# Kernel optimization log

Measured on AMD Instinct MI355X. Metric: run time of the kernel, lower is better.

The kernel has to match this reference:

```python
import jax, jax.numpy as jnp
import numpy as np
import math

B, S, HID = 1, 2048, 4096
NH, NKV, HD = 32, 8, 128
N_REP = NH // NKV
ROPE_THETA = 10000.0


def setup_inputs() -> dict:
    key = jax.random.key(0)
    ks = jax.random.split(key, 5)
    hidden_states = jax.random.normal(ks[0], (B, S, HID), dtype=jnp.float32)
    # additive causal mask: 0 on/below diagonal, -1e9 above
    causal = jnp.triu(jnp.full((S, S), -1e9, dtype=jnp.float32), k=1)
    attention_mask = causal[None, None, :, :]
    wq = jax.random.normal(ks[1], (HID, NH * HD), dtype=jnp.float32) * 0.02
    wk = jax.random.normal(ks[2], (HID, NKV * HD), dtype=jnp.float32) * 0.02
    wv = jax.random.normal(ks[3], (HID, NKV * HD), dtype=jnp.float32) * 0.02
    wo = jax.random.normal(ks[4], (NH * HD, HID), dtype=jnp.float32) * 0.02
    return {"hidden_states": hidden_states, "attention_mask": attention_mask,
            "wq": wq, "wk": wk, "wv": wv, "wo": wo}


def _rope_cos_sin(seq_len, head_dim, base, dtype):
    inv_freq = 1.0 / (base ** (jnp.arange(0, head_dim, 2, dtype=jnp.float32) / head_dim))
    t = jnp.arange(seq_len, dtype=jnp.float32)
    freqs = jnp.outer(t, inv_freq)          # [S, HD/2]
    emb = jnp.concatenate([freqs, freqs], axis=-1)  # [S, HD]
    return jnp.cos(emb).astype(dtype), jnp.sin(emb).astype(dtype)


def _rotate_interleaved(x):
    # pairs (x0,x1) -> (-x1, x0), interleaved (matches torch stack/reshape trick)
    xp = x.reshape(*x.shape[:-1], -1, 2)
    return jnp.stack([-xp[..., 1], xp[..., 0]], axis=-1).reshape(x.shape)


def reference(hidden_states, attention_mask, wq, wk, wv, wo):
    b, s, _ = hidden_states.shape
    q = (hidden_states @ wq).reshape(b, s, NH, HD).transpose(0, 2, 1, 3)   # [B,NH,S,HD]
    k = (hidden_states @ wk).reshape(b, s, NKV, HD).transpose(0, 2, 1, 3)  # [B,NKV,S,HD]
    v = (hidden_states @ wv).reshape(b, s, NKV, HD).transpose(0, 2, 1, 3)

    cos, sin = _rope_cos_sin(s, HD, ROPE_THETA, hidden_states.dtype)
    cos = cos[None, None, :, :]  # broadcast over batch and heads
    sin = sin[None, None, :, :]
    q = q * cos + _rotate_interleaved(q) * sin
    k = k * cos + _rotate_interleaved(k) * sin

    # repeat_kv: [B,NKV,S,HD] -> [B,NH,S,HD]
    k = jnp.repeat(k, N_REP, axis=1)
    v = jnp.repeat(v, N_REP, axis=1)

    scores = jnp.einsum('bhqd,bhkd->bhqk', q, k) / math.sqrt(HD)
    scores = scores + attention_mask
    attn = jax.nn.softmax(scores.astype(jnp.float32), axis=-1).astype(q.dtype)
    out = jnp.einsum('bhqk,bhkd->bhqd', attn, v)          # [B,NH,S,HD]
    out = out.transpose(0, 2, 1, 3).reshape(b, s, NH * HD)
    return out @ wo
```

## Files before the change

### kernel.cpp

```cpp
#include <hip/hip_runtime.h>

#define S_LEN 2048
#define HID 4096
#define NH 32
#define NKV 8
#define HD 128
#define KVW 1024
#define NQKV 6144

typedef _Float16 f16;
typedef _Float16 f16x8 __attribute__((ext_vector_type(8)));
typedef _Float16 f16x4 __attribute__((ext_vector_type(4)));
typedef float f32x4 __attribute__((ext_vector_type(4)));
typedef float f32x16 __attribute__((ext_vector_type(16)));
typedef unsigned int u32;
typedef u32 u32x4 __attribute__((ext_vector_type(4)));

__device__ __forceinline__ void gll16(const void* g, void* lds) {
  __builtin_amdgcn_global_load_lds((const __attribute__((address_space(1))) void*)g,
                                   (__attribute__((address_space(3))) void*)lds, 16, 0, 0);
}

template<int N> __device__ __forceinline__ void vmwait() {
  if constexpr (N == 0) asm volatile("s_waitcnt vmcnt(0)" ::: "memory");
  else if constexpr (N == 2) asm volatile("s_waitcnt vmcnt(2)" ::: "memory");
  else if constexpr (N == 3) asm volatile("s_waitcnt vmcnt(3)" ::: "memory");
  else if constexpr (N == 4) asm volatile("s_waitcnt vmcnt(4)" ::: "memory");
  else if constexpr (N == 6) asm volatile("s_waitcnt vmcnt(6)" ::: "memory");
  else static_assert(N == 0, "add vmcnt case");
}

__global__ void k_cast(const float* __restrict__ src, f16* __restrict__ dst) {
  size_t i = ((size_t)blockIdx.x * blockDim.x + threadIdx.x) * 8;
  float4 a = *(const float4*)(src + i);
  float4 b = *(const float4*)(src + i + 4);
  f16x8 o = { (f16)a.x, (f16)a.y, (f16)a.z, (f16)a.w,
              (f16)b.x, (f16)b.y, (f16)b.z, (f16)b.w };
  *(f16x8*)(dst + i) = o;
}

__global__ void k_trig(float4* __restrict__ trig) {
  int id = blockIdx.x * blockDim.x + threadIdx.x;
  int s = id >> 6, i = id & 63;
  int j0 = 2 * i, j1 = 2 * i + 1;
  float f0 = powf(10000.f, -(float)(j0 & 63) / 64.f);
  float f1 = powf(10000.f, -(float)(j1 & 63) / 64.f);
  float a0 = (float)s * f0, a1 = (float)s * f1;
  trig[id] = make_float4(cosf(a0), cosf(a1), sinf(a0), sinf(a1));
}

__global__ __launch_bounds__(256) void k_wprep(
    const float* __restrict__ wq, const float* __restrict__ wk,
    const float* __restrict__ wv, const float* __restrict__ wo,
    f16* __restrict__ Wt, f16* __restrict__ Wot)
{
  __shared__ float tile[32][33];
  int bid = blockIdx.x;
  const float* src; f16* dst; int N; int r;
  if (bid < 16384)      { src = wq; dst = Wt;                          N = 4096; r = bid; }
  else if (bid < 20480) { src = wk; dst = Wt + (size_t)4096 * 4096;    N = 1024; r = bid - 16384; }
  else if (bid < 24576) { src = wv; dst = Wt + (size_t)5120 * 4096;    N = 1024; r = bid - 20480; }
  else                  { src = wo; dst = Wot;                         N = 4096; r = bid - 24576; }
  int tpr = N >> 5;
  int kb = (r / tpr) * 32, nb = (r % tpr) * 32;
  int t = threadIdx.x;
  {
    int kl = t >> 3, ng = t & 7;
    float4 v = *(const float4*)(src + (size_t)(kb + kl) * N + nb + ng * 4);
    tile[kl][ng * 4 + 0] = v.x; tile[kl][ng * 4 + 1] = v.y;
    tile[kl][ng * 4 + 2] = v.z; tile[kl][ng * 4 + 3] = v.w;
  }
  __syncthreads();
  {
    int nl = t >> 3, kg = t & 7;
    f16x4 o = { (f16)tile[kg * 4 + 0][nl], (f16)tile[kg * 4 + 1][nl],
                (f16)tile[kg * 4 + 2][nl], (f16)tile[kg * 4 + 3][nl] };
    *(f16x4*)(dst + (size_t)(nb + nl) * HID + kb + kg * 4) = o;
  }
}

extern __shared__ char smem[];

template<int MODE, int MF, int NF, int WM, int WN>
__global__ __launch_bounds__(WM * WN * 64, 2) void k_gemm4(
    const f16* __restrict__ A, const f16* __restrict__ Bt,
    f16* __restrict__ Qr, f16* __restrict__ Kr, f16* __restrict__ Vt,
    const float4* __restrict__ trig, float* __restrict__ Cout)
{
  constexpr int NTHR = WM * WN * 64;
  constexpr int BM = WM * MF * 16;
  constexpr int BN = WN * NF * 16;
  constexpr int ABYTES = BM * 128;
  constexpr int BBYTES = BN * 128;
  constexpr int RPC = NTHR / 8;
  constexpr int ACALLS = BM / RPC;
  constexpr int BCALLS = BN / RPC;
  constexpr int NT = 64;

  const int tid = threadIdx.x, ln = tid & 63, w = tid >> 6;
  const int la = ln & 15, lg = ln >> 4;
  const int wr = w / WN, wc = w % WN;

  int bx, by;
  {
    int b = blockIdx.y * gridDim.x + blockIdx.x;
    int cx = gridDim.x >> 3;
    int xcd = b & 7, rr = b >> 3;
    bx = xcd * cx + (rr % cx);
    by = rr / cx;
  }
  const int m0 = by * BM, n0 = bx * BN;

  const char* asrc[ACALLS];
  const char* bsrc[BCALLS];
  int adst[ACALLS > BCALLS ? ACALLS : BCALLS];
#pragma unroll
  for (int c = 0; c < ACALLS; ++c) {
    int r = c * RPC + (tid >> 3);
    int g = (tid & 7) ^ (r & 7);
    asrc[c] = (const char*)A + ((size_t)(m0 + r) * HID + (size_t)g * 8) * 2;
    adst[c] = c * NTHR * 16 + tid * 16;
  }
#pragma unroll
  for (int c = 0; c < BCALLS; ++c) {
    int r = c * RPC + (tid >> 3);
    int g = (tid & 7) ^ (r & 7);
    bsrc[c] = (const char*)Bt + ((size_t)(n0 + (r >= BN ? r - BN : r)) * HID + (size_t)g * 8) * 2;
  }

  char* const Bbase = smem + 2 * ABYTES;
  f32x4 acc[MF][NF] = {};

#pragma unroll
  for (int c = 0; c < ACALLS; ++c) gll16(asrc[c], smem + adst[c]);
#pragma unroll
  for (int c = 0; c < BCALLS; ++c) gll16(bsrc[c], Bbase + adst[c]);
#pragma unroll
  for (int c = 0; c < BCALLS; ++c) gll16(bsrc[c] + 128, Bbase + 1 * BBYTES + adst[c]);
#pragma unroll
  for (int c = 0; c < BCALLS; ++c) gll16(bsrc[c] + 256, Bbase + 2 * BBYTES + adst[c]);
  vmwait<2 * BCALLS>();
  __builtin_amdgcn_s_barrier();

  for (int t = 0; t < NT; ++t) {
    if (t + 1 < NT) {
      char* sa = smem + ((t + 1) & 1) * ABYTES;
#pragma unroll
      for (int c = 0; c < ACALLS; ++c) gll16(asrc[c] + (size_t)(t + 1) * 128, sa + adst[c]);
    }
    if (t + 3 < NT) {
      char* sb = Bbase + ((t + 3) & 3) * BBYTES;
#pragma unroll
      for (int c = 0; c < BCALLS; ++c) gll16(bsrc[c] + (size_t)(t + 3) * 128, sb + adst[c]);
    }
    const char* sa = smem + (t & 1) * ABYTES;
    const char* sb = Bbase + (t & 3) * BBYTES;
#pragma unroll
    for (int ks = 0; ks < 2; ++ks) {
      f16x8 af[MF], bf[NF];
#pragma unroll
      for (int i = 0; i < MF; ++i) {
        int rl = wr * MF * 16 + i * 16 + la;
        af[i] = *(const f16x8*)(sa + rl * 128 + (((ks * 4 + lg) ^ (rl & 7)) * 16));
      }
#pragma unroll
      for (int n = 0; n < NF; ++n) {
        int rb = wc * NF * 16 + n * 16 + la;
        bf[n] = *(const f16x8*)(sb + rb * 128 + (((ks * 4 + lg) ^ (rb & 7)) * 16));
      }
      __builtin_amdgcn_s_setprio(1);
#pragma unroll
      for (int i = 0; i < MF; ++i)
#pragma unroll
        for (int n = 0; n < NF; ++n)
          acc[i][n] = __builtin_amdgcn_mfma_f32_16x16x32_f16(af[i], bf[n], acc[i][n], 0, 0, 0);
      __builtin_amdgcn_s_setprio(0);
    }
    if (t < NT - 3)      vmwait<BCALLS>();
    else if (t < NT - 1) vmwait<0>();
    if (t < NT - 1) __builtin_amdgcn_s_barrier();
  }

#pragma unroll
  for (int mi = 0; mi < MF; ++mi) {
#pragma unroll
    for (int nf = 0; nf < NF; ++nf) {
      f32x4 fr = acc[mi][nf];
      int n = n0 + wc * NF * 16 + nf * 16 + la;
      int mr = m0 + wr * MF * 16 + mi * 16 + lg * 4;
      if (MODE == 0) {
        if (n < HID + KVW) {
          int d = n & 127;
#pragma unroll
          for (int r = 0; r < 4; ++r) {
            float v = fr[r];
            float p = __shfl_xor(v, 1);
            float4 tc = trig[(size_t)(mr + r) * 64 + (d >> 1)];
            float cv = (d & 1) ? tc.y : tc.x;
            float sv = (d & 1) ? tc.w : tc.z;
            float o = v * cv + ((d & 1) ? p : -p) * sv;
            if (n < HID) Qr[(size_t)(mr + r) * HID + n] = (f16)o;
            else         Kr[(size_t)(mr + r) * KVW + (n - HID)] = (f16)o;
          }
        } else {
          int nv = n - (HID + KVW);
          f16x4 o4 = { (f16)fr[0], (f16)fr[1], (f16)fr[2], (f16)fr[3] };
          *(f16x4*)(Vt + (size_t)nv * S_LEN + mr) = o4;
        }
      } else {
#pragma unroll
        for (int r = 0; r < 4; ++r)
          Cout[(size_t)(mr + r) * HID + n] = fr[r];
      }
    }
  }
}

#define KBYTES (64 * 128 * 2)
#define VBYTES (128 * 64 * 2)

__global__ __launch_bounds__(256, 2) void k_attn(
    const f16* __restrict__ Qr, const f16* __restrict__ Kr, const f16* __restrict__ Vt,
    f16* __restrict__ AO)
{
  int bid = blockIdx.x;
  int h, c;
  if (bid < 256) { h = bid >> 3; c = bid & 7; }
  else           { int t = bid - 256; h = t >> 3; c = 15 - (t & 7); }
  const int hkv = h >> 2;
  const int q0c = c * 128;
  const int NT = 2 * c + 2;

  __shared__ char KV[2][KBYTES + VBYTES];

  const int tid = threadIdx.x;
  const int ln = tid & 63, w = tid >> 6;
  const int q = ln & 31;
  const int hi = ln >> 5;
  const int qg = q0c + w * 32 + q;

  size_t ksrc[4], vsrc[4];
  int kdo[4], vdo[4];
#pragma unroll
  for (int j = 0; j < 4; ++j) {
    int kc = w * 4 + j;
    int kr = kc * 4 + (ln >> 4);
    ksrc[j] = ((size_t)kr * KVW + hkv * HD) * 2 + (size_t)(((ln & 15) ^ (kr & 7)) * 16);
    kdo[j] = kc * 1024;
    int vc = w * 4 + j;
    int d = vc * 8 + (ln >> 3);
    vsrc[j] = ((size_t)(hkv * HD + d) * S_LEN) * 2 + (size_t)(((ln & 7) ^ (d & 7)) * 16);
    vdo[j] = KBYTES + vc * 1024;
  }

  f16x8 qf[8];
  {
    const f16* qrow = Qr + (size_t)qg * HID + h * HD + hi * 8;
#pragma unroll
    for (int ks = 0; ks < 8; ++ks) qf[ks] = *(const f16x8*)(qrow + ks * 16);
  }

  f32x16 ot[4] = {};
  float m2 = -3.0e38f, l = 0.f;
  const float K2 = 0.12753256471f;

  int buf = 0;
#pragma unroll
  for (int j = 0; j < 4; ++j) {
    gll16((const char*)Kr + ksrc[j], &KV[0][kdo[j]]);
    gll16((const char*)Vt + vsrc[j], &KV[0][vdo[j]]);
  }

  for (int jt = 0; jt < NT; ++jt) {
    __syncthreads();
    if (jt + 1 < NT) {
      size_t ko = (size_t)(jt + 1) * 64 * KVW * 2;
      size_t vo = (size_t)(jt + 1) * 64 * 2;
#pragma unroll
      for (int j = 0; j < 4; ++j) {
        gll16((const char*)Kr + ksrc[j] + ko, &KV[buf ^ 1][kdo[j]]);
        gll16((const char*)Vt + vsrc[j] + vo, &KV[buf ^ 1][vdo[j]]);
      }
    }
    const int j0 = jt * 64;
    if (j0 <= q0c + w * 32 + 31) {
      const f16* Kb = (const f16*)&KV[buf][0];
      const f16* Vb = (const f16*)&KV[buf][KBYTES];
      f32x16 s0 = {}, s1 = {};
#pragma unroll
      for (int ks = 0; ks < 8; ++ks) {
        int cc = ((ks * 2 + hi) ^ (q & 7)) * 8;
        f16x8 k0 = *(const f16x8*)(Kb + q * 128 + cc);
        f16x8 k1 = *(const f16x8*)(Kb + (q + 32) * 128 + cc);
        s0 = __builtin_amdgcn_mfma_f32_32x32x16_f16(k0, qf[ks], s0, 0, 0, 0);
        s1 = __builtin_amdgcn_mfma_f32_32x32x16_f16(k1, qf[ks], s1, 0, 0, 0);
      }
      const bool nm = (j0 + 63 > q0c + w * 32);
      float p0[16], p1[16];
      float mx = -3.0e38f;
#pragma unroll
      for (int r = 0; r < 16; ++r) {
        float a = s0[r], b = s1[r];
        if (nm) {
          int kvb = j0 + (r & 3) + 8 * (r >> 2) + 4 * hi;
          if (kvb > qg) a = -3.0e38f;
          if (kvb + 32 > qg) b = -3.0e38f;
        }
        p0[r] = a; p1[r] = b;
        mx = fmaxf(mx, fmaxf(a, b));
      }
      mx = fmaxf(mx, __shfl_xor(mx, 32));
      float m2c = mx * K2;
      int defer = (m2c <= m2 + 11.0f);
      if (!__all(defer)) {
        float m2n = fmaxf(m2, m2c);
        float corr = exp2f(m2 - m2n);
        m2 = m2n; l *= corr;
#pragma unroll
        for (int t = 0; t < 4; ++t)
#pragma unroll
          for (int r = 0; r < 16; ++r) ot[t][r] *= corr;
      }
      float sum = 0.f;
#pragma unroll
      for (int r = 0; r < 16; ++r) {
        p0[r] = exp2f(__builtin_fmaf(p0[r], K2, -m2));
        p1[r] = exp2f(__builtin_fmaf(p1[r], K2, -m2));
        sum += p0[r] + p1[r];
      }
      l += sum + __shfl_xor(sum, 32);
      u32 pw0[8], pw1[8];
#pragma unroll
      for (int t = 0; t < 8; ++t) {
        pw0[t] = __builtin_bit_cast(u32, __builtin_amdgcn_cvt_pkrtz(p0[2 * t], p0[2 * t + 1]));
        pw1[t] = __builtin_bit_cast(u32, __builtin_amdgcn_cvt_pkrtz(p1[2 * t], p1[2 * t + 1]));
      }
      f16x8 pf[4];
#pragma unroll
      for (int ch = 0; ch < 2; ++ch) {
        const u32* pw = ch ? pw1 : pw0;
        u32 sx[8];
#pragma unroll
        for (int t = 0; t < 8; ++t) sx[t] = (u32)__shfl_xor((int)pw[t], 32);
        u32x4 fa = { hi ? sx[2] : pw[0], hi ? sx[3] : pw[1],
                     hi ? pw[2] : sx[0], hi ? pw[3] : sx[1] };
        u32x4 fb = { hi ? sx[6] : pw[4], hi ? sx[7] : pw[5],
                     hi ? pw[6] : sx[4], hi ? pw[7] : sx[5] };
        pf[ch * 2 + 0] = __builtin_bit_cast(f16x8, fa);
        pf[ch * 2 + 1] = __builtin_bit_cast(f16x8, fb);
      }
#pragma unroll
      for (int dt = 0; dt < 4; ++dt) {
        int d = dt * 32 + q;
#pragma unroll
        for (int f = 0; f < 4; ++f) {
          f16x8 vf = *(const f16x8*)(Vb + d * 64 + (((f * 2 + hi) ^ (q & 7)) * 8));
          ot[dt] = __builtin_amdgcn_mfma_f32_32x32x16_f16(vf, pf[f], ot[dt], 0, 0, 0);
        }
      }
    }
    buf ^= 1;
  }

  __syncthreads();
  char* scr = &KV[0][0] + w * 8192;
  float inv = 1.f / l;
#pragma unroll
  for (int dt = 0; dt < 4; ++dt) {
#pragma unroll
    for (int rg = 0; rg < 4; ++rg) {
      u32 wa = __builtin_bit_cast(u32, __builtin_amdgcn_cvt_pkrtz(ot[dt][rg * 4 + 0] * inv, ot[dt][rg * 4 + 1] * inv));
      u32 wb = __builtin_bit_cast(u32, __builtin_amdgcn_cvt_pkrtz(ot[dt][rg * 4 + 2] * inv, ot[dt][rg * 4 + 3] * inv));
      int byte = q * 256 + (((dt * 4 + rg) ^ (q & 7)) * 16) + hi * 8;
      u32* p = (u32*)(scr + byte);
      p[0] = wa; p[1] = wb;
    }
  }
  asm volatile("s_waitcnt lgkmcnt(0)" ::: "memory");
#pragma unroll
  for (int ps = 0; ps < 8; ++ps) {
    int qr = ps * 4 + (ln >> 4);
    int ck = (ln & 15) ^ (qr & 7);
    f16x8 v = *(const f16x8*)(scr + qr * 256 + ck * 16);
    *(f16x8*)(AO + (size_t)(q0c + w * 32 + qr) * HID + h * HD + (ln & 15) * 8) = v;
  }
}

extern "C" void kernel_launch(void* const* d_in, const int* in_sizes, int n_in,
                              void* d_out, int out_size, void* d_ws, size_t ws_size,
                              hipStream_t stream) {
  const float* hs = (const float*)d_in[0];
  const float* wq = (const float*)d_in[2];
  const float* wk = (const float*)d_in[3];
  const float* wv = (const float*)d_in[4];
  const float* wo = (const float*)d_in[5];
  float* out = (float*)d_out;

  char* ws = (char*)d_ws;
  size_t off = 0;
  auto alloc = [&](size_t b) { char* p = ws + off; off += (b + 255) & ~(size_t)255; return p; };
  f16* Hh   = (f16*)alloc((size_t)S_LEN * HID * 2);
  f16* Wt   = (f16*)alloc((size_t)NQKV * HID * 2);
  float4* trig = (float4*)alloc((size_t)S_LEN * 64 * sizeof(float4));
  f16* Qrp  = (f16*)alloc((size_t)S_LEN * HID * 2);
  f16* Krp  = (f16*)alloc((size_t)S_LEN * KVW * 2);
  f16* Vtp  = (f16*)alloc((size_t)KVW * S_LEN * 2);
  f16* AO   = (f16*)alloc((size_t)S_LEN * HID * 2);
  f16* Wot  = (f16*)alloc((size_t)HID * HID * 2);

  hipFuncSetAttribute((const void*)k_gemm4<0, 8, 3, 2, 4>,
                      hipFuncAttributeMaxDynamicSharedMemorySize, 163840);
  hipFuncSetAttribute((const void*)k_gemm4<1, 8, 2, 2, 4>,
                      hipFuncAttributeMaxDynamicSharedMemorySize, 131072);

  k_cast<<<(S_LEN * HID) / (256 * 8), 256, 0, stream>>>(hs, Hh);
  k_trig<<<(S_LEN * 64) / 256, 256, 0, stream>>>(trig);
  k_wprep<<<40960, 256, 0, stream>>>(wq, wk, wv, wo, Wt, Wot);
  k_gemm4<0, 8, 3, 2, 4><<<dim3(NQKV / 192, S_LEN / 256), 512, 163840, stream>>>(
      Hh, Wt, Qrp, Krp, Vtp, trig, nullptr);
  k_attn<<<dim3(512), 256, 0, stream>>>(Qrp, Krp, Vtp, AO);
  k_gemm4<1, 8, 2, 2, 4><<<dim3(HID / 128, S_LEN / 256), 512, 131072, stream>>>(
      AO, Wot, nullptr, nullptr, nullptr, nullptr, out);
}
```

Measured before the change: 322.5 us.

## Add finer-grained pipelined QKV GEMM kernel and fuse prep kernels into one launch

Replaces the templated QKV projection GEMM with a dedicated kernel that splits each K-tile into half-k stages. It uses a 4-slot A ring and a 3-slot B ring, interleaves global-to-LDS loads between MFMA sub-blocks with more barriers, and remaps blocks per XCD for locality. It also merges the cast, trig and weight-transpose kernels into a single launch to cut launch overhead. LDS per block drops, but the extra barriers and finer vmcnt waits may stall waves.

```diff
diff --git a/kernel.cpp b/kernel.cpp
--- a/kernel.cpp
+++ b/kernel.cpp
@@ -26,36 +26,44 @@
   else if constexpr (N == 2) asm volatile("s_waitcnt vmcnt(2)" ::: "memory");
   else if constexpr (N == 3) asm volatile("s_waitcnt vmcnt(3)" ::: "memory");
   else if constexpr (N == 4) asm volatile("s_waitcnt vmcnt(4)" ::: "memory");
+  else if constexpr (N == 5) asm volatile("s_waitcnt vmcnt(5)" ::: "memory");
   else if constexpr (N == 6) asm volatile("s_waitcnt vmcnt(6)" ::: "memory");
+  else if constexpr (N == 7) asm volatile("s_waitcnt vmcnt(7)" ::: "memory");
+  else if constexpr (N == 8) asm volatile("s_waitcnt vmcnt(8)" ::: "memory");
   else static_assert(N == 0, "add vmcnt case");
 }
-
-__global__ void k_cast(const float* __restrict__ src, f16* __restrict__ dst) {
-  size_t i = ((size_t)blockIdx.x * blockDim.x + threadIdx.x) * 8;
-  float4 a = *(const float4*)(src + i);
-  float4 b = *(const float4*)(src + i + 4);
-  f16x8 o = { (f16)a.x, (f16)a.y, (f16)a.z, (f16)a.w,
-              (f16)b.x, (f16)b.y, (f16)b.z, (f16)b.w };
-  *(f16x8*)(dst + i) = o;
-}
-
-__global__ void k_trig(float4* __restrict__ trig) {
-  int id = blockIdx.x * blockDim.x + threadIdx.x;
-  int s = id >> 6, i = id & 63;
-  int j0 = 2 * i, j1 = 2 * i + 1;
-  float f0 = powf(10000.f, -(float)(j0 & 63) / 64.f);
-  float f1 = powf(10000.f, -(float)(j1 & 63) / 64.f);
-  float a0 = (float)s * f0, a1 = (float)s * f1;
-  trig[id] = make_float4(cosf(a0), cosf(a1), sinf(a0), sinf(a1));
-}
-
-__global__ __launch_bounds__(256) void k_wprep(
-    const float* __restrict__ wq, const float* __restrict__ wk,
-    const float* __restrict__ wv, const float* __restrict__ wo,
-    f16* __restrict__ Wt, f16* __restrict__ Wot)
+#define LGKM0 asm volatile("s_waitcnt lgkmcnt(0)" ::: "memory")
+#define BAR() __builtin_amdgcn_s_barrier()
+
+__global__ __launch_bounds__(256) void k_prep(
+    const float* __restrict__ hs, const float* __restrict__ wq,
+    const float* __restrict__ wk, const float* __restrict__ wv,
+    const float* __restrict__ wo,
+    f16* __restrict__ Hh, f16* __restrict__ Wt, f16* __restrict__ Wot,
+    float4* __restrict__ trig)
 {
   __shared__ float tile[32][33];
   int bid = blockIdx.x;
+  int t = threadIdx.x;
+  if (bid >= 40960) {
+    int b2 = bid - 40960;
+    if (b2 < 4096) {
+      size_t i = ((size_t)b2 * 256 + t) * 8;
+      float4 a = *(const float4*)(hs + i);
+      float4 b = *(const float4*)(hs + i + 4);
+      f16x8 o = { (f16)a.x, (f16)a.y, (f16)a.z, (f16)a.w,
+                  (f16)b.x, (f16)b.y, (f16)b.z, (f16)b.w };
+      *(f16x8*)(Hh + i) = o;
+    } else {
+      int id = (b2 - 4096) * 256 + t;
+      int s = id >> 6, i = id & 63;
+      float f0 = powf(10000.f, -(float)((2 * i) & 63) / 64.f);
+      float f1 = powf(10000.f, -(float)((2 * i + 1) & 63) / 64.f);
+      float a0 = (float)s * f0, a1 = (float)s * f1;
+      trig[id] = make_float4(cosf(a0), cosf(a1), sinf(a0), sinf(a1));
+    }
+    return;
+  }
   const float* src; f16* dst; int N; int r;
   if (bid < 16384)      { src = wq; dst = Wt;                          N = 4096; r = bid; }
   else if (bid < 20480) { src = wk; dst = Wt + (size_t)4096 * 4096;    N = 1024; r = bid - 16384; }
@@ -63,7 +71,6 @@
   else                  { src = wo; dst = Wot;                         N = 4096; r = bid - 24576; }
   int tpr = N >> 5;
   int kb = (r / tpr) * 32, nb = (r % tpr) * 32;
-  int t = threadIdx.x;
   {
     int kl = t >> 3, ng = t & 7;
     float4 v = *(const float4*)(src + (size_t)(kb + kl) * N + nb + ng * 4);
@@ -80,6 +87,151 @@
 }
 
 extern __shared__ char smem[];
+
+__global__ __launch_bounds__(512, 2) void k_gemm8(
+    const f16* __restrict__ A, const f16* __restrict__ Bt,
+    f16* __restrict__ Qr, f16* __restrict__ Kr, f16* __restrict__ Vt,
+    const float4* __restrict__ trig)
+{
+  constexpr int BN = 192;
+  constexpr int NF = 3;
+  constexpr int BCALLS = BN / 64;
+  constexpr int BBYTES = BN * 128;
+  constexpr int TI = 4 + BCALLS;
+  constexpr int W_END = TI, W_MID = TI + 1;
+  constexpr int NT = 64;
+
+  const int tid = threadIdx.x, ln = tid & 63, w = tid >> 6;
+  const int la = ln & 15, lg = ln >> 4;
+  const int wr = w >> 2, wc = w & 3;
+
+  int bx, by;
+  {
+    int b = blockIdx.y * gridDim.x + blockIdx.x;
+    int cx = gridDim.x >> 3;
+    int xcd = b & 7, rr = b >> 3;
+    bx = xcd * cx + (rr % cx);
+    by = rr / cx;
+  }
+  const int m0 = by * 256, n0 = bx * BN;
+
+  const char* asrcA[2];
+#pragma unroll
+  for (int c = 0; c < 2; ++c) {
+    int row = c * 128 + (tid >> 2);
+    int sg = (tid & 3) ^ ((row >> 1) & 3);
+    asrcA[c] = (const char*)A + ((size_t)(m0 + row) * HID) * 2 + (size_t)sg * 16;
+  }
+  const char* bsrcB[BCALLS];
+#pragma unroll
+  for (int c = 0; c < BCALLS; ++c) {
+    int row = c * 64 + (tid >> 3);
+    int g = (tid & 7) ^ (row & 7);
+    bsrcB[c] = (const char*)Bt + ((size_t)(n0 + row) * HID) * 2 + (size_t)g * 16;
+  }
+  char* const Bbase = smem + 65536;
+  const int d16 = tid * 16;
+
+  auto stA = [&](int t, int h) {
+    char* b = smem + (((2 * t + h) & 3) * 16384) + d16;
+    size_t off = (size_t)t * 128 + h * 64;
+    gll16(asrcA[0] + off, b); gll16(asrcA[1] + off, b + 8192);
+  };
+  auto stB = [&](int t, int c) {
+    char* b = Bbase + (t % 3) * BBYTES + c * 8192 + d16;
+    gll16(bsrcB[c] + (size_t)t * 128, b);
+  };
+  f16x8 af[4], bf[NF];
+  auto ldA = [&](int t, int mh, int ks) {
+    const char* sb = smem + (((2 * t + ks) & 3) * 16384);
+#pragma unroll
+    for (int i = 0; i < 4; ++i) {
+      int rl = wr * 128 + mh * 64 + i * 16 + la;
+      af[i] = *(const f16x8*)(sb + rl * 64 + ((lg ^ ((rl >> 1) & 3)) * 16));
+    }
+  };
+  auto ldB = [&](int t, int ks) {
+    const char* sb = Bbase + (t % 3) * BBYTES;
+#pragma unroll
+    for (int n = 0; n < NF; ++n) {
+      int rb = wc * (NF * 16) + n * 16 + la;
+      bf[n] = *(const f16x8*)(sb + rb * 128 + (((ks * 4 + lg) ^ (rb & 7)) * 16));
+    }
+  };
+
+  f32x4 acc[8][NF] = {};
+
+#define MM12(MH)                                                                      \
+  __builtin_amdgcn_s_setprio(1);                                                      \
+  _Pragma("unroll")                                                                   \
+  for (int i = 0; i < 4; ++i)                                                         \
+    _Pragma("unroll")                                                                 \
+    for (int n = 0; n < NF; ++n)                                                      \
+      acc[(MH)*4 + i][n] =                                                            \
+        __builtin_amdgcn_mfma_f32_16x16x32_f16(af[i], bf[n], acc[(MH)*4 + i][n], 0, 0, 0); \
+  __builtin_amdgcn_s_setprio(0);
+
+  stA(0, 0); stA(0, 1);
+  for (int c = 0; c < BCALLS; ++c) stB(0, c);
+  stA(1, 0);
+  for (int c = 0; c < BCALLS; ++c) stB(1, c);
+  vmwait<BCALLS + 2>();
+  BAR();
+
+  for (int t = 0; t < NT; ++t) {
+    ldA(t, 0, 0); ldB(t, 0);
+    if (t + 1 < NT) stA(t + 1, 1);
+    BAR(); LGKM0;
+    MM12(0);
+    BAR();
+    ldA(t, 1, 0);
+    if (t + 2 < NT) stB(t + 2, 0);
+    BAR(); LGKM0;
+    MM12(1);
+    if (t < NT - 2) vmwait<W_MID>(); else vmwait<0>();
+    BAR();
+    ldA(t, 0, 1); ldB(t, 1);
+    if (t + 2 < NT) { stA(t + 2, 0); stB(t + 2, 1); }
+    BAR(); LGKM0;
+    MM12(0);
+    BAR();
+    ldA(t, 1, 1);
+    if (t + 2 < NT) stB(t + 2, 2);
+    BAR(); LGKM0;
+    MM12(1);
+    if (t < NT - 2) vmwait<W_END>(); else vmwait<0>();
+    BAR();
+  }
+#undef MM12
+
+#pragma unroll
+  for (int mi = 0; mi < 8; ++mi) {
+#pragma unroll
+    for (int nf = 0; nf < NF; ++nf) {
+      f32x4 fr = acc[mi][nf];
+      int n = n0 + wc * (NF * 16) + nf * 16 + la;
+      int mr = m0 + wr * 128 + mi * 16 + lg * 4;
+      if (n < HID + KVW) {
+        int d = n & 127;
+#pragma unroll
+        for (int r = 0; r < 4; ++r) {
+          float v = fr[r];
+          float p = __shfl_xor(v, 1);
+          float4 tc = trig[(size_t)(mr + r) * 64 + (d >> 1)];
+          float cv = (d & 1) ? tc.y : tc.x;
+          float sv = (d & 1) ? tc.w : tc.z;
+          float o = v * cv + ((d & 1) ? p : -p) * sv;
+          if (n < HID) Qr[(size_t)(mr + r) * HID + n] = (f16)o;
+          else         Kr[(size_t)(mr + r) * KVW + (n - HID)] = (f16)o;
+        }
+      } else {
+        int nv = n - (HID + KVW);
+        f16x4 o4 = { (f16)fr[0], (f16)fr[1], (f16)fr[2], (f16)fr[3] };
+        *(f16x4*)(Vt + (size_t)nv * S_LEN + mr) = o4;
+      }
+    }
+  }
+}
 
 template<int MODE, int MF, int NF, int WM, int WN>
 __global__ __launch_bounds__(WM * WN * 64, 2) void k_gemm4(
@@ -188,26 +340,7 @@
       f32x4 fr = acc[mi][nf];
       int n = n0 + wc * NF * 16 + nf * 16 + la;
       int mr = m0 + wr * MF * 16 + mi * 16 + lg * 4;
-      if (MODE == 0) {
-        if (n < HID + KVW) {
-          int d = n & 127;
-#pragma unroll
-          for (int r = 0; r < 4; ++r) {
-            float v = fr[r];
-            float p = __shfl_xor(v, 1);
-            float4 tc = trig[(size_t)(mr + r) * 64 + (d >> 1)];
-            float cv = (d & 1) ? tc.y : tc.x;
-            float sv = (d & 1) ? tc.w : tc.z;
-            float o = v * cv + ((d & 1) ? p : -p) * sv;
-            if (n < HID) Qr[(size_t)(mr + r) * HID + n] = (f16)o;
-            else         Kr[(size_t)(mr + r) * KVW + (n - HID)] = (f16)o;
-          }
-        } else {
-          int nv = n - (HID + KVW);
-          f16x4 o4 = { (f16)fr[0], (f16)fr[1], (f16)fr[2], (f16)fr[3] };
-          *(f16x4*)(Vt + (size_t)nv * S_LEN + mr) = o4;
-        }
-      } else {
+      if (MODE == 1) {
 #pragma unroll
         for (int r = 0; r < 4; ++r)
           Cout[(size_t)(mr + r) * HID + n] = fr[r];
@@ -408,16 +541,14 @@
   f16* AO   = (f16*)alloc((size_t)S_LEN * HID * 2);
   f16* Wot  = (f16*)alloc((size_t)HID * HID * 2);
 
-  hipFuncSetAttribute((const void*)k_gemm4<0, 8, 3, 2, 4>,
-                      hipFuncAttributeMaxDynamicSharedMemorySize, 163840);
+  hipFuncSetAttribute((const void*)k_gemm8,
+                      hipFuncAttributeMaxDynamicSharedMemorySize, 139264);
   hipFuncSetAttribute((const void*)k_gemm4<1, 8, 2, 2, 4>,
                       hipFuncAttributeMaxDynamicSharedMemorySize, 131072);
 
-  k_cast<<<(S_LEN * HID) / (256 * 8), 256, 0, stream>>>(hs, Hh);
-  k_trig<<<(S_LEN * 64) / 256, 256, 0, stream>>>(trig);
-  k_wprep<<<40960, 256, 0, stream>>>(wq, wk, wv, wo, Wt, Wot);
-  k_gemm4<0, 8, 3, 2, 4><<<dim3(NQKV / 192, S_LEN / 256), 512, 163840, stream>>>(
-      Hh, Wt, Qrp, Krp, Vtp, trig, nullptr);
+  k_prep<<<45568, 256, 0, stream>>>(hs, wq, wk, wv, wo, Hh, Wt, Wot, trig);
+  k_gemm8<<<dim3(NQKV / 192, S_LEN / 256), 512, 139264, stream>>>(
+      Hh, Wt, Qrp, Krp, Vtp, trig);
   k_attn<<<dim3(512), 256, 0, stream>>>(Qrp, Krp, Vtp, AO);
   k_gemm4<1, 8, 2, 2, 4><<<dim3(HID / 128, S_LEN / 256), 512, 131072, stream>>>(
       AO, Wot, nullptr, nullptr, nullptr, nullptr, out);
```

After: 323.4 us. About the same (+0.3%).
